# Kernel optimization log

Hardware: AMD Instinct MI355X
Metric: run time of the kernel (lower is better)

## Reference

```python
import jax, jax.numpy as jnp
import numpy as np
from jax import lax


def _lstm_dir(x_gates, Whh, bhh, reverse):
    # x_gates: (B,T,4H) = x @ Wih.T + bih, precomputed for all timesteps
    B, T, G = x_gates.shape
    H = G // 4

    def step(carry, xg):
        h, c = carry
        g = xg + h @ Whh.T + bhh
        i, f, gg, o = jnp.split(g, 4, axis=-1)  # PyTorch gate order i,f,g,o
        c = jax.nn.sigmoid(f) * c + jax.nn.sigmoid(i) * jnp.tanh(gg)
        h = jax.nn.sigmoid(o) * jnp.tanh(c)
        return (h, c), h

    xs = jnp.swapaxes(x_gates, 0, 1)  # (T,B,4H)
    if reverse:
        xs = xs[::-1]
    init = (jnp.zeros((B, H), x_gates.dtype), jnp.zeros((B, H), x_gates.dtype))
    _, hs = lax.scan(step, init, xs)
    if reverse:
        hs = hs[::-1]
    return jnp.swapaxes(hs, 0, 1)  # (B,T,H)


def _forward(embeddings, mask,
             enc_Wih_f, enc_Whh_f, enc_bih_f, enc_bhh_f,
             enc_Wih_b, enc_Whh_b, enc_bih_b, enc_bhh_b,
             attn_W, attn_b, tag_embed,
             dec_Wih, dec_Whh, dec_bih, dec_bhh,
             Wout, bout):
    B, T, D = embeddings.shape
    maskf = mask.astype(embeddings.dtype)

    # --- bidirectional encoder ---
    xg_f = jnp.einsum('btd,gd->btg', embeddings, enc_Wih_f) + enc_bih_f
    xg_b = jnp.einsum('btd,gd->btg', embeddings, enc_Wih_b) + enc_bih_b
    out_f = _lstm_dir(xg_f, enc_Whh_f, enc_bhh_f, False)
    out_b = _lstm_dir(xg_b, enc_Whh_b, enc_bhh_b, True)
    output = jnp.concatenate([out_f, out_b], axis=-1) * maskf[:, :, None]  # (B,T,2H)

    lengths = mask.sum(axis=1) - 1
    last_output = output[jnp.arange(B), lengths]  # (B,2H)

    def attend(v):
        # AllenNLP BilinearAttention: softmax(v @ W @ M^T + b), then * mask
        sc = jnp.einsum('bd,de,bte->bt', v, attn_W, output) + attn_b
        return jax.nn.softmax(sc, axis=-1) * maskf

    context0 = jnp.einsum('bt,btd->bd', attend(last_output), output)  # (B,2H)

    Hd = output.shape[-1]          # decoder hidden = 2H
    E = tag_embed.shape[1]         # tag embedding dim (== hidden_size)
    h0 = jnp.zeros((B, Hd), embeddings.dtype)
    c0 = jnp.zeros((B, Hd), embeddings.dtype)

    def step(carry, xt):
        h, c, context, last_tag = carry
        aligned, i = xt
        emb = jnp.where(i == 0,
                        jnp.zeros((B, E), embeddings.dtype),
                        tag_embed[last_tag])
        dec_input = jnp.concatenate([emb, context, aligned], axis=-1)  # (B, E+4H)
        g = dec_input @ dec_Wih.T + dec_bih + h @ dec_Whh.T + dec_bhh
        ii, f, gg, o = jnp.split(g, 4, axis=-1)
        c = jax.nn.sigmoid(f) * c + jax.nn.sigmoid(ii) * jnp.tanh(gg)
        h = jax.nn.sigmoid(o) * jnp.tanh(c)
        concated = jnp.concatenate([h, context], axis=-1)  # (B,4H)
        score = concated @ Wout.T + bout                   # (B,V)
        new_context = jnp.einsum('bt,btd->bd', attend(h), output)
        last_tag = jnp.argmax(score, axis=-1).astype(jnp.int32)
        return (h, c, new_context, last_tag), score

    xs = (jnp.swapaxes(output, 0, 1), jnp.arange(T))
    init = (h0, c0, context0, jnp.zeros((B,), jnp.int32))
    _, scores = lax.scan(step, init, xs)  # (T,B,V)
    return jnp.swapaxes(scores, 0, 1)     # (B,T,V) slot logits


def setup_inputs() -> dict:
    key = jax.random.key(0)
    B, T, D, H, E, V = 32, 64, 512, 512, 512, 2048
    H2 = 2 * H
    dec_in = E + 2 * H2  # tag_emb + context(2H) + aligned(2H)
    ks = jax.random.split(key, 20)
    s = 0.02
    f32 = jnp.float32
    return {
        'embeddings': jax.random.normal(ks[0], (B, T, D), f32),
        'mask': jnp.ones((B, T), jnp.int32),
        'enc_Wih_f': jax.random.normal(ks[1], (4 * H, D), f32) * s,
        'enc_Whh_f': jax.random.normal(ks[2], (4 * H, H), f32) * s,
        'enc_bih_f': jax.random.normal(ks[3], (4 * H,), f32) * s,
        'enc_bhh_f': jax.random.normal(ks[4], (4 * H,), f32) * s,
        'enc_Wih_b': jax.random.normal(ks[5], (4 * H, D), f32) * s,
        'enc_Whh_b': jax.random.normal(ks[6], (4 * H, H), f32) * s,
        'enc_bih_b': jax.random.normal(ks[7], (4 * H,), f32) * s,
        'enc_bhh_b': jax.random.normal(ks[8], (4 * H,), f32) * s,
        'attn_W': jax.random.normal(ks[9], (H2, H2), f32) * s,
        'attn_b': jax.random.normal(ks[10], (), f32) * s,
        'tag_embed': jax.random.normal(ks[11], (V, E), f32) * s,
        'dec_Wih': jax.random.normal(ks[12], (4 * H2, dec_in), f32) * s,
        'dec_Whh': jax.random.normal(ks[13], (4 * H2, H2), f32) * s,
        'dec_bih': jax.random.normal(ks[14], (4 * H2,), f32) * s,
        'dec_bhh': jax.random.normal(ks[15], (4 * H2,), f32) * s,
        'Wout': jax.random.normal(ks[16], (V, 2 * H2), f32) * s,
        'bout': jax.random.normal(ks[17], (V,), f32) * s,
    }


def reference(embeddings, mask,
              enc_Wih_f, enc_Whh_f, enc_bih_f, enc_bhh_f,
              enc_Wih_b, enc_Whh_b, enc_bih_b, enc_bhh_b,
              attn_W, attn_b, tag_embed,
              dec_Wih, dec_Whh, dec_bih, dec_bhh,
              Wout, bout):
    return _forward(embeddings, mask,
                    enc_Wih_f, enc_Whh_f, enc_bih_f, enc_bhh_f,
                    enc_Wih_b, enc_Whh_b, enc_bih_b, enc_bhh_b,
                    attn_W, attn_b, tag_embed,
                    dec_Wih, dec_Whh, dec_bih, dec_bhh,
                    Wout, bout)
```

## Files before the change

### kernel.cpp

```cpp
#include <hip/hip_runtime.h>

#define B   32
#define T   64
#define D   512
#define H   512
#define H2  1024
#define G4  4096
#define V   2048
#define DEC_IN 2560

__device__ __forceinline__ float sigm(float x) { return 1.f / (1.f + expf(-x)); }

__device__ __forceinline__ unsigned fenc(float f) {
  unsigned u = __float_as_uint(f);
  return (u & 0x80000000u) ? ~u : (u | 0x80000000u);
}

__device__ __forceinline__ void st_wt(float* p, float v) {
  __hip_atomic_store(p, v, __ATOMIC_RELAXED, __HIP_MEMORY_SCOPE_AGENT);
}

__device__ __forceinline__ void pbar(unsigned* slots, unsigned* flags, int myid, int nblk) {
  __syncthreads();
  if (threadIdx.x == 0)
    __hip_atomic_store(slots + myid, 1u, __ATOMIC_RELAXED, __HIP_MEMORY_SCOPE_AGENT);
  if (myid == 0) {
    for (int s = threadIdx.x; s < nblk; s += 256) {
      while (!__hip_atomic_load(slots + s, __ATOMIC_RELAXED, __HIP_MEMORY_SCOPE_AGENT))
        __builtin_amdgcn_s_sleep(1);
    }
    __syncthreads();
    if (threadIdx.x < 16)
      __hip_atomic_store(flags + threadIdx.x*16, 1u, __ATOMIC_RELAXED, __HIP_MEMORY_SCOPE_AGENT);
  }
  if (threadIdx.x == 0) {
    unsigned* f = flags + (myid & 15)*16;
    while (!__hip_atomic_load(f, __ATOMIC_RELAXED, __HIP_MEMORY_SCOPE_AGENT))
      __builtin_amdgcn_s_sleep(1);
    (void)__hip_atomic_load(f, __ATOMIC_ACQUIRE, __HIP_MEMORY_SCOPE_AGENT);
  }
  __syncthreads();
}

__device__ __forceinline__ void pbar_na(unsigned* slots, unsigned* flags, int myid, int nblk) {
  __syncthreads();
  if (threadIdx.x == 0)
    __hip_atomic_store(slots + myid, 1u, __ATOMIC_RELAXED, __HIP_MEMORY_SCOPE_AGENT);
  if (myid == 0) {
    for (int s = threadIdx.x; s < nblk; s += 256) {
      while (!__hip_atomic_load(slots + s, __ATOMIC_RELAXED, __HIP_MEMORY_SCOPE_AGENT))
        __builtin_amdgcn_s_sleep(1);
    }
    __syncthreads();
    if (threadIdx.x < 16)
      __hip_atomic_store(flags + threadIdx.x*16, 1u, __ATOMIC_RELAXED, __HIP_MEMORY_SCOPE_AGENT);
  }
  if (threadIdx.x == 0) {
    unsigned* f = flags + (myid & 15)*16;
    while (!__hip_atomic_load(f, __ATOMIC_RELAXED, __HIP_MEMORY_SCOPE_AGENT))
      __builtin_amdgcn_s_sleep(1);
  }
  __syncthreads();
}

__global__ __launch_bounds__(256) void gemm_nt(
    const float* __restrict__ A, int lda,
    const float* __restrict__ W, int ldw,
    float* __restrict__ C, int ldc,
    const float* __restrict__ bias0, const float* __restrict__ bias1,
    int K)
{
  __shared__ float As[8][132];
  __shared__ float Bs[8][132];
  const int tid = threadIdx.x;
  const int nb = blockIdx.x * 128;
  const int mb = blockIdx.y * 128;
  const int tx = tid & 15;
  const int ty = tid >> 4;
  float acc[8][8] = {};

  const int am = tid >> 1, ak = (tid & 1) * 4;
  const float* aptr = A + (size_t)(mb + am) * lda + ak;
  const float* bptr = W + (size_t)(nb + am) * ldw + ak;

  for (int k0 = 0; k0 < K; k0 += 8) {
    float4 av = *(const float4*)(aptr + k0);
    float4 bv = *(const float4*)(bptr + k0);
    As[ak+0][am] = av.x; As[ak+1][am] = av.y; As[ak+2][am] = av.z; As[ak+3][am] = av.w;
    Bs[ak+0][am] = bv.x; Bs[ak+1][am] = bv.y; Bs[ak+2][am] = bv.z; Bs[ak+3][am] = bv.w;
    __syncthreads();
    #pragma unroll
    for (int k = 0; k < 8; ++k) {
      float4 a0 = *(const float4*)&As[k][ty*8];
      float4 a1 = *(const float4*)&As[k][ty*8+4];
      float4 b0 = *(const float4*)&Bs[k][tx*8];
      float4 b1 = *(const float4*)&Bs[k][tx*8+4];
      float avv[8] = {a0.x,a0.y,a0.z,a0.w,a1.x,a1.y,a1.z,a1.w};
      float bvv[8] = {b0.x,b0.y,b0.z,b0.w,b1.x,b1.y,b1.z,b1.w};
      #pragma unroll
      for (int i = 0; i < 8; ++i)
        #pragma unroll
        for (int j = 0; j < 8; ++j)
          acc[i][j] += avv[i]*bvv[j];
    }
    __syncthreads();
  }
  float b8[8];
  #pragma unroll
  for (int j = 0; j < 8; ++j) {
    float bvv = 0.f;
    if (bias0) bvv += bias0[nb + tx*8 + j];
    if (bias1) bvv += bias1[nb + tx*8 + j];
    b8[j] = bvv;
  }
  #pragma unroll
  for (int i = 0; i < 8; ++i) {
    float4 o0, o1;
    o0.x = acc[i][0]+b8[0]; o0.y = acc[i][1]+b8[1]; o0.z = acc[i][2]+b8[2]; o0.w = acc[i][3]+b8[3];
    o1.x = acc[i][4]+b8[4]; o1.y = acc[i][5]+b8[5]; o1.z = acc[i][6]+b8[6]; o1.w = acc[i][7]+b8[7];
    size_t idx = (size_t)(mb + ty*8 + i) * ldc + nb + tx*8;
    *(float4*)&C[idx]     = o0;
    *(float4*)&C[idx + 4] = o1;
  }
}

__device__ void attend_slice(int ab, int aslice, const float* __restrict__ hvec,
                             float* __restrict__ ctxdst,
                             const float* __restrict__ outbuf, const float* __restrict__ projo,
                             const int* __restrict__ mask, float* scratch, int tid)
{
  float* scp = scratch;
  float* scv = scratch + 256;
  float* p2  = scratch + 320;
  const int tq = tid >> 2, dq = tid & 3;
  const float4* hv = (const float4*)(hvec + dq*256);
  const float4* pv = (const float4*)(projo + (size_t)(ab*T + tq)*H2 + dq*256);
  float p = 0.f;
  #pragma unroll 8
  for (int k4 = 0; k4 < 64; ++k4) {
    float4 a = hv[k4], q = pv[k4];
    p += a.x*q.x + a.y*q.y + a.z*q.z + a.w*q.w;
  }
  scp[tid] = p;
  __syncthreads();
  if (tid < 64) {
    float v = scp[tid*4] + scp[tid*4+1] + scp[tid*4+2] + scp[tid*4+3];
    float mx = v;
    #pragma unroll
    for (int d = 32; d; d >>= 1) mx = fmaxf(mx, __shfl_xor(mx, d, 64));
    float e = expf(v - mx);
    float sm = e;
    #pragma unroll
    for (int d = 32; d; d >>= 1) sm += __shfl_xor(sm, d, 64);
    scv[tid] = e * (1.f / sm) * (float)mask[ab*T + tid];
  }
  __syncthreads();
  {
    const int dl = tid & 127, th = tid >> 7;
    const int dg = aslice*128 + dl;
    float acc = 0.f;
    #pragma unroll 8
    for (int q = 0; q < 32; ++q) {
      int tt = th*32 + q;
      acc += scv[tt] * outbuf[(size_t)(ab*T + tt)*H2 + dg];
    }
    if (th == 1) p2[dl] = acc;
    __syncthreads();
    if (th == 0) st_wt(&ctxdst[dg*32 + ab], acc + p2[dl]);
  }
}

__global__ __launch_bounds__(256, 1) void encoder_persistent(
    const float* __restrict__ xg_f, const float* __restrict__ xg_b,
    const float* __restrict__ Whh_f, const float* __restrict__ Whh_b,
    const int* __restrict__ mask,
    float* __restrict__ hencT,
    float* __restrict__ outbuf,
    unsigned* __restrict__ eslots, unsigned* __restrict__ eflags)
{
  __shared__ float S_lds[9216];
  __shared__ float pacc[2048];
  __shared__ float g_lds[512];
  const int blk = blockIdx.x, tid = threadIdx.x;
  const int lane = tid & 63, wv = tid >> 6;
  const int dir = blk >> 7, nd = blk & 127;
  const int hibase = nd * 4;
  const int jj = tid & 7, kk = tid >> 3;
  const int kkl = lane >> 3;
  const float* xg  = dir ? xg_b : xg_f;
  const float* Whh = dir ? Whh_b : Whh_f;
  float* hbase = hencT + dir * 32768;
  float* Sw = S_lds + wv*2304;

  float wge[2][16];
  #pragma unroll
  for (int p = 0; p < 2; ++p) {
    int jl = jj*2 + p;
    int j = (jl>>2)*512 + hibase + (jl&3);
    #pragma unroll
    for (int sc = 0; sc < 4; ++sc)
      #pragma unroll
      for (int i = 0; i < 4; ++i)
        wge[p][sc*4+i] = Whh[(size_t)j*512 + sc*128 + i*32 + kk];
  }
  float c_reg = 0.f;
  const int lr = lane >> 1, halfc = (lane & 1) * 16;
  const int grow = (lr >> 3)*32 + 8*wv + (lr & 7);

  for (int tt = 0; tt < 64; ++tt) {
    const int t = dir ? (63 - tt) : tt;
    const float* hc = hbase + (tt & 1) * 16384;
    float* hn = hbase + ((tt + 1) & 1) * 16384;

    float a0[32], a1[32];
    #pragma unroll
    for (int q = 0; q < 32; ++q) { a0[q] = 0.f; a1[q] = 0.f; }

    float4 r0, r1, r2, r3;
    {
      const float4* p = (const float4*)(hc + grow*32 + halfc);
      r0 = p[0]; r1 = p[1]; r2 = p[2]; r3 = p[3];
      float* d = Sw + lr*36 + halfc;
      *(float4*)d = r0; *(float4*)(d+4) = r1; *(float4*)(d+8) = r2; *(float4*)(d+12) = r3;
    }
    #pragma unroll
    for (int sc = 0; sc < 4; ++sc) {
      if (sc < 3) {
        const float4* p = (const float4*)(hc + ((sc+1)*128 + grow)*32 + halfc);
        r0 = p[0]; r1 = p[1]; r2 = p[2]; r3 = p[3];
      }
      const float* Sb = Sw + (sc & 1)*1152;
      #pragma unroll
      for (int i = 0; i < 4; ++i) {
        const float* sp = Sb + (i*8 + kkl)*36;
        float w0 = wge[0][sc*4+i], w1 = wge[1][sc*4+i];
        #pragma unroll
        for (int q = 0; q < 8; ++q) {
          float4 s4 = *(const float4*)(sp + q*4);
          a0[q*4+0] += w0*s4.x; a0[q*4+1] += w0*s4.y; a0[q*4+2] += w0*s4.z; a0[q*4+3] += w0*s4.w;
          a1[q*4+0] += w1*s4.x; a1[q*4+1] += w1*s4.y; a1[q*4+2] += w1*s4.z; a1[q*4+3] += w1*s4.w;
        }
      }
      if (sc < 3) {
        float* d = Sw + ((sc+1) & 1)*1152 + lr*36 + halfc;
        *(float4*)d = r0; *(float4*)(d+4) = r1; *(float4*)(d+8) = r2; *(float4*)(d+12) = r3;
      }
    }
    #pragma unroll
    for (int dd = 8; dd <= 32; dd <<= 1) {
      #pragma unroll
      for (int q = 0; q < 32; ++q) {
        a0[q] += __shfl_down(a0[q], dd, 64);
        a1[q] += __shfl_down(a1[q], dd, 64);
      }
    }
    if (lane < 8) {
      float* pw = &pacc[wv*512 + lane*64];
      #pragma unroll
      for (int q = 0; q < 32; ++q) { pw[q] = a0[q]; pw[32+q] = a1[q]; }
    }
    __syncthreads();
    #pragma unroll
    for (int r = 0; r < 2; ++r) {
      int o = tid + r*256;
      int jl = o >> 5, b = o & 31;
      int off = (jl>>1)*64 + (jl&1)*32 + b;
      float v = pacc[off] + pacc[512+off] + pacc[1024+off] + pacc[1536+off];
      v += xg[(size_t)(b*T + t)*2048 + (jl>>2)*512 + hibase + (jl&3)];
      g_lds[jl*32 + b] = v;
    }
    __syncthreads();
    if (tid < 128) {
      int hil = tid >> 5, b = tid & 31;
      float gi = g_lds[(0*4+hil)*32 + b];
      float gf = g_lds[(1*4+hil)*32 + b];
      float gg = g_lds[(2*4+hil)*32 + b];
      float go = g_lds[(3*4+hil)*32 + b];
      c_reg = sigm(gf)*c_reg + sigm(gi)*tanhf(gg);
      float h = sigm(go)*tanhf(c_reg);
      int hi = hibase + hil;
      st_wt(&hn[hi*32 + b], h);
      st_wt(&outbuf[(size_t)(b*T + t)*H2 + dir*512 + hi], h * (float)mask[b*T + t]);
    }
    pbar(eslots + (dir*64 + tt)*128, eflags + (dir*64 + tt)*256, nd, 128);
  }
}

#define GROW1(lr) (8*wv + ((lr) < 8 ? (lr) : 24 + (lr)))
#define GROW2(lr) (16*wv + (lr))
#define SLDG(qq, s) { int krr = (s)*64 + GROW1(lrow); \
  const float* bs = (krr < 1024) ? (hTc + krr*32) : (ctxc + (krr-1024)*32); \
  qq##a = *(const float4*)(bs + scol2); qq##b = *(const float4*)(bs + scol2 + 4); }
#define SLDS(qq, s) { int krr = (s)*64 + GROW2(lrow); \
  const float* bs = (krr < 1024) ? (hTn + krr*32) : (ctxc + (krr-1024)*32); \
  qq##a = *(const float4*)(bs + scol2); qq##b = *(const float4*)(bs + scol2 + 4); }
#define STW(qq, BUF) { float* d = Sw + (BUF)*576 + lrow*36 + scol2; \
  *(float4*)d = qq##a; *(float4*)(d+4) = qq##b; }
#define COMPG(sl, BUF) { const float* Sb = Sw + (BUF)*576; \
  _Pragma("unroll") for (int i = 0; i < 2; ++i) { \
    float w0 = Wg[jl0*2052 + (sl)*64 + i*32 + kkg]; \
    float w1 = Wg[jl1*2052 + (sl)*64 + i*32 + kkg]; \
    const float* sp = Sb + (i*8 + kkl)*36; \
    _Pragma("unroll") for (int q = 0; q < 8; ++q) { \
      float4 s4 = *(const float4*)(sp + q*4); \
      a0[q*4+0] += w0*s4.x; a0[q*4+1] += w0*s4.y; a0[q*4+2] += w0*s4.z; a0[q*4+3] += w0*s4.w; \
      a1[q*4+0] += w1*s4.x; a1[q*4+1] += w1*s4.y; a1[q*4+2] += w1*s4.z; a1[q*4+3] += w1*s4.w; } } }
#define COMPS(sl, BUF) { const float* sp = Sw + (BUF)*576 + lrow*36; \
  float w0 = ws0[sl], w1 = ws1[sl]; \
  _Pragma("unroll") for (int q = 0; q < 8; ++q) { \
    float4 s4 = *(const float4*)(sp + q*4); \
    a0[q*4+0] += w0*s4.x; a0[q*4+1] += w0*s4.y; a0[q*4+2] += w0*s4.z; a0[q*4+3] += w0*s4.w; \
    a1[q*4+0] += w1*s4.x; a1[q*4+1] += w1*s4.y; a1[q*4+2] += w1*s4.z; a1[q*4+3] += w1*s4.w; } }

__global__ __launch_bounds__(256, 1) void decoder_persistent(
    const float* __restrict__ basep, const float* __restrict__ tagp,
    const float* __restrict__ dWhh,  const float* __restrict__ dWih,
    const float* __restrict__ Wout,  const float* __restrict__ bout,
    const float* __restrict__ projo, const float* __restrict__ outbuf,
    const int* __restrict__ mask,
    float* __restrict__ hbufs,
    float* __restrict__ cbufs,
    float* __restrict__ rbufs,
    const float* __restrict__ zeroh,
    unsigned long long* __restrict__ argslot,
    unsigned* __restrict__ dslots, unsigned* __restrict__ dflags,
    float* __restrict__ out)
{
  extern __shared__ float dyn[];
  float* Wg    = dyn;
  float* S2    = dyn + 32832;
  float* pacc  = dyn + 37440;
  float* g_lds = dyn + 39488;

  const int blk = blockIdx.x, tid = threadIdx.x;
  const int lane = tid & 63, wv = tid >> 6;
  const int hibase = blk * 4;
  const int jj = lane & 7, kkl = lane >> 3;
  const int kkg = 8*wv + kkl;
  const int jl0 = jj*2, jl1 = jj*2 + 1;
  const int vv = tid & 3, kq = tid >> 2;
  const int vbase = blk * 8;
  const int lrow = lane >> 2, scol2 = (lane & 3) * 8;
  const int ab = blk & 31, aslice = blk >> 5;
  float* Sw = S2 + wv*1152;

  for (int jl = 0; jl < 16; ++jl) {
    int j = (jl>>2)*1024 + hibase + (jl&3);
    #pragma unroll
    for (int r = 0; r < 2; ++r) {
      int c = tid*4 + r*1024;
      float4 w;
      if (c < 1024) w = *(const float4*)(dWhh + (size_t)j*1024 + c);
      else          w = *(const float4*)(dWih + (size_t)j*2560 + 512 + (c - 1024));
      *(float4*)&Wg[jl*2052 + c] = w;
    }
  }
  float ws0[32], ws1[32];
  {
    int v0 = vbase + vv*2;
    #pragma unroll
    for (int s2 = 0; s2 < 32; ++s2) {
      ws0[s2] = Wout[(size_t)(v0+0)*2048 + s2*64 + kq];
      ws1[s2] = Wout[(size_t)(v0+1)*2048 + s2*64 + kq];
    }
  }

  float c_reg = 0.f;
  int bslot = 0;

  {
    int len = -1;
    for (int i = 0; i < T; ++i) len += mask[ab*T + i];
    attend_slice(ab, aslice, outbuf + (size_t)(ab*T + len)*H2, cbufs,
                 outbuf, projo, mask, pacc, tid);
  }
  pbar_na(dslots + (bslot)*256, dflags + (bslot)*256, blk, 256); bslot++;

  for (int t = 0; t < T; ++t) {
    const float* hTc  = (t == 0) ? zeroh : (hbufs + (size_t)(t-1)*32768);
    float*       hTn  = hbufs + (size_t)t*32768;
    const float* ctxc = cbufs + (size_t)t*32768;
    float*       ctxn = cbufs + (size_t)(t+1)*32768;
    float*       hrw  = rbufs + (size_t)t*32768;

    const int b_own = tid & 31;
    const int jlA = tid >> 5, jlB = jlA + 8;
    const int jA = (jlA>>2)*1024 + hibase + (jlA&3);
    const int jB = (jlB>>2)*1024 + hibase + (jlB&3);
    float extA = basep[(size_t)(b_own*T + t)*G4 + jA];
    float extB = basep[(size_t)(b_own*T + t)*G4 + jB];
    if (t > 0) {
      unsigned long long sl64 = __hip_atomic_load(&argslot[((t+2)%3)*32 + b_own],
                                                  __ATOMIC_RELAXED, __HIP_MEMORY_SCOPE_AGENT);
      unsigned tg = ~(unsigned)sl64;
      extA += tagp[(size_t)tg*G4 + jA];
      extB += tagp[(size_t)tg*G4 + jB];
    }

    float a0[32], a1[32];
    #pragma unroll
    for (int q = 0; q < 32; ++q) { a0[q] = 0.f; a1[q] = 0.f; }
    {
      float4 q0a,q0b,q1a,q1b,q2a,q2b,q3a,q3b;
      SLDG(q0, 0) SLDG(q1, 1) SLDG(q2, 2) SLDG(q3, 3)
      STW(q0, 0)
      for (int g = 0; g < 8; ++g) {
        const int sl = g*4;
        if (sl+4 < 32) SLDG(q0, sl+4)
        COMPG(sl, 0)
        STW(q1, 1)
        if (sl+5 < 32) SLDG(q1, sl+5)
        COMPG(sl+1, 1)
        STW(q2, 0)
        if (sl+6 < 32) SLDG(q2, sl+6)
        COMPG(sl+2, 0)
        STW(q3, 1)
        if (sl+7 < 32) SLDG(q3, sl+7)
        COMPG(sl+3, 1)
        if (sl+4 < 32) STW(q0, 0)
      }
    }
    #pragma unroll
    for (int dd = 8; dd <= 32; dd <<= 1) {
      #pragma unroll
      for (int q = 0; q < 32; ++q) {
        a0[q] += __shfl_down(a0[q], dd, 64);
        a1[q] += __shfl_down(a1[q], dd, 64);
      }
    }
    if (lane < 8) {
      float* pw = &pacc[wv*512 + lane*64];
      #pragma unroll
      for (int q = 0; q < 32; ++q) { pw[q] = a0[q]; pw[32+q] = a1[q]; }
    }
    __syncthreads();
    #pragma unroll
    for (int r = 0; r < 2; ++r) {
      int o = tid + r*256;
      int jl = o >> 5, b = o & 31;
      int off = (jl>>1)*64 + (jl&1)*32 + b;
      float vsum = pacc[off] + pacc[512+off] + pacc[1024+off] + pacc[1536+off];
      vsum += (r == 0) ? extA : extB;
      g_lds[jl*32 + b] = vsum;
    }
    __syncthreads();
    if (tid < 128) {
      int hil = tid >> 5, b = tid & 31;
      float gi = g_lds[(0*4+hil)*32 + b];
      float gf = g_lds[(1*4+hil)*32 + b];
      float gg = g_lds[(2*4+hil)*32 + b];
      float go = g_lds[(3*4+hil)*32 + b];
      c_reg = sigm(gf)*c_reg + sigm(gi)*tanhf(gg);
      float h = sigm(go)*tanhf(c_reg);
      int hi = hibase + hil;
      st_wt(&hTn[hi*32 + b], h);
      st_wt(&hrw[b*1024 + hi], h);
    }
    pbar_na(dslots + (bslot)*256, dflags + (bslot)*256, blk, 256); bslot++;

    #pragma unroll
    for (int q = 0; q < 32; ++q) { a0[q] = 0.f; a1[q] = 0.f; }
    {
      float4 q0a,q0b,q1a,q1b,q2a,q2b,q3a,q3b;
      SLDS(q0, 0) SLDS(q1, 1) SLDS(q2, 2) SLDS(q3, 3)
      STW(q0, 0)
      #pragma unroll
      for (int g = 0; g < 8; ++g) {
        const int sl = g*4;
        if (sl+4 < 32) SLDS(q0, sl+4)
        COMPS(sl, 0)
        STW(q1, 1)
        if (sl+5 < 32) SLDS(q1, sl+5)
        COMPS(sl+1, 1)
        STW(q2, 0)
        if (sl+6 < 32) SLDS(q2, sl+6)
        COMPS(sl+2, 0)
        STW(q3, 1)
        if (sl+7 < 32) SLDS(q3, sl+7)
        COMPS(sl+3, 1)
        if (sl+4 < 32) STW(q0, 0)
      }
    }
    #pragma unroll
    for (int dd = 4; dd <= 32; dd <<= 1) {
      #pragma unroll
      for (int q = 0; q < 32; ++q) {
        a0[q] += __shfl_down(a0[q], dd, 64);
        a1[q] += __shfl_down(a1[q], dd, 64);
      }
    }
    if (lane < 4) {
      float* pw = &pacc[wv*256 + lane*64];
      #pragma unroll
      for (int q = 0; q < 32; ++q) { pw[q] = a0[q]; pw[32+q] = a1[q]; }
    }
    __syncthreads();
    {
      int vl = tid & 7, b = tid >> 3;
      int off = (vl>>1)*64 + (vl&1)*32 + b;
      float s = pacc[off] + pacc[256+off] + pacc[512+off] + pacc[768+off];
      s += bout[vbase + vl];
      st_wt(&out[(size_t)(b*T + t)*V + vbase + vl], s);
      g_lds[vl*32 + b] = s;
    }
    __syncthreads();
    if (tid < 32) {
      int b = tid;
      float best = g_lds[b]; int bi = 0;
      #pragma unroll
      for (int vl = 1; vl < 8; ++vl) {
        float s = g_lds[vl*32 + b];
        if (s > best) { best = s; bi = vl; }
      }
      unsigned long long e = ((unsigned long long)fenc(best) << 32)
                           | (unsigned long long)(unsigned)(~(unsigned)(vbase + bi));
      atomicMax(&argslot[(t%3)*32 + b], e);
    } else if (blk == 0 && tid >= 32 && tid < 64) {
      __hip_atomic_store(&argslot[((t+1)%3)*32 + (tid - 32)], 0ull,
                         __ATOMIC_RELAXED, __HIP_MEMORY_SCOPE_AGENT);
    }
    if (t < 63) {
      __syncthreads();
      attend_slice(ab, aslice, hrw + ab*1024, ctxn, outbuf, projo, mask, pacc, tid);
    }
    pbar_na(dslots + (bslot)*256, dflags + (bslot)*256, blk, 256); bslot++;
  }
}

extern "C" void kernel_launch(void* const* d_in, const int* in_sizes, int n_in,
                              void* d_out, int out_size, void* d_ws, size_t ws_size,
                              hipStream_t stream)
{
  (void)in_sizes; (void)n_in; (void)out_size; (void)ws_size;
  const float* emb    = (const float*)d_in[0];
  const int*   mask   = (const int*)d_in[1];
  const float* Wih_f  = (const float*)d_in[2];
  const float* Whh_f  = (const float*)d_in[3];
  const float* bih_f  = (const float*)d_in[4];
  const float* bhh_f  = (const float*)d_in[5];
  const float* Wih_b  = (const float*)d_in[6];
  const float* Whh_b  = (const float*)d_in[7];
  const float* bih_b  = (const float*)d_in[8];
  const float* bhh_b  = (const float*)d_in[9];
  const float* attnW  = (const float*)d_in[10];
  const float* tagemb = (const float*)d_in[12];
  const float* dWih   = (const float*)d_in[13];
  const float* dWhh   = (const float*)d_in[14];
  const float* dbih   = (const float*)d_in[15];
  const float* dbhh   = (const float*)d_in[16];
  const float* Wout   = (const float*)d_in[17];
  const float* bout   = (const float*)d_in[18];
  float* out = (float*)d_out;

  float* ws = (float*)d_ws;
  float* xg_f   = ws + 0;
  float* xg_b   = ws + 4194304;
  float* hbufs  = ws + 0;
  float* cbufs  = ws + 2097152;
  float* rbufs  = ws + 4227072;
  float* outbuf = ws + 8388608;
  float* projo  = ws + 10485760;
  float* basep  = ws + 12582912;
  float* tagp   = ws + 20971520;
  float* zeroh  = ws + 29360128;
  float* hencT  = ws + 29523968;
  unsigned long long* argslot = (unsigned long long*)(ws + 29589504);
  unsigned* dslots = (unsigned*)(ws + 29589696);
  unsigned* dflags = (unsigned*)(ws + 29622720);
  unsigned* eslots = (unsigned*)(ws + 29655744);
  unsigned* eflags = (unsigned*)(ws + 29672128);

  (void)hipFuncSetAttribute((const void*)decoder_persistent,
                            hipFuncAttributeMaxDynamicSharedMemorySize, 160000);

  hipMemsetAsync((void*)(ws + 29360128), 0, (size_t)(29704896 - 29360128) * sizeof(float), stream);

  gemm_nt<<<dim3(16, 16), 256, 0, stream>>>(emb, 512, Wih_f, 512, xg_f, 2048, bih_f, bhh_f, 512);
  gemm_nt<<<dim3(16, 16), 256, 0, stream>>>(emb, 512, Wih_b, 512, xg_b, 2048, bih_b, bhh_b, 512);
  gemm_nt<<<dim3(32, 16), 256, 0, stream>>>(tagemb, 512, dWih, DEC_IN, tagp, G4, nullptr, nullptr, 512);
  encoder_persistent<<<256, 256, 0, stream>>>(xg_f, xg_b, Whh_f, Whh_b, mask, hencT, outbuf, eslots, eflags);
  gemm_nt<<<dim3(8, 16), 256, 0, stream>>>(outbuf, H2, attnW, H2, projo, H2, nullptr, nullptr, H2);
  gemm_nt<<<dim3(32, 16), 256, 0, stream>>>(outbuf, H2, dWih + 1536, DEC_IN, basep, G4, dbih, dbhh, H2);
  decoder_persistent<<<256, 256, 160000, stream>>>(basep, tagp, dWhh, dWih, Wout, bout,
                                                   projo, outbuf, mask, hbufs, cbufs, rbufs, zeroh,
                                                   argslot, dslots, dflags, out);
}
```

Before: 4.548 ms.

## Use per-timestep encoder hidden buffers with non-acquire barrier; prefetch GEMM tiles

The encoder now writes each timestep's hidden state into its own buffer instead of ping-ponging between two. That removes write-after-read hazards, which lets the grid barrier drop its acquire load (pbar_na). Separately, the tiled GEMM register-prefetches the next K slice while computing the current one, hiding global load latency. The per-timestep buffers reuse the basep region, which is only written after the encoder finishes. They also use more memory and rely on the weaker barrier still ordering the relaxed atomic stores correctly.

```diff
diff --git a/kernel.cpp b/kernel.cpp
--- a/kernel.cpp
+++ b/kernel.cpp
@@ -18,28 +18,6 @@
 
 __device__ __forceinline__ void st_wt(float* p, float v) {
   __hip_atomic_store(p, v, __ATOMIC_RELAXED, __HIP_MEMORY_SCOPE_AGENT);
-}
-
-__device__ __forceinline__ void pbar(unsigned* slots, unsigned* flags, int myid, int nblk) {
-  __syncthreads();
-  if (threadIdx.x == 0)
-    __hip_atomic_store(slots + myid, 1u, __ATOMIC_RELAXED, __HIP_MEMORY_SCOPE_AGENT);
-  if (myid == 0) {
-    for (int s = threadIdx.x; s < nblk; s += 256) {
-      while (!__hip_atomic_load(slots + s, __ATOMIC_RELAXED, __HIP_MEMORY_SCOPE_AGENT))
-        __builtin_amdgcn_s_sleep(1);
-    }
-    __syncthreads();
-    if (threadIdx.x < 16)
-      __hip_atomic_store(flags + threadIdx.x*16, 1u, __ATOMIC_RELAXED, __HIP_MEMORY_SCOPE_AGENT);
-  }
-  if (threadIdx.x == 0) {
-    unsigned* f = flags + (myid & 15)*16;
-    while (!__hip_atomic_load(f, __ATOMIC_RELAXED, __HIP_MEMORY_SCOPE_AGENT))
-      __builtin_amdgcn_s_sleep(1);
-    (void)__hip_atomic_load(f, __ATOMIC_ACQUIRE, __HIP_MEMORY_SCOPE_AGENT);
-  }
-  __syncthreads();
 }
 
 __device__ __forceinline__ void pbar_na(unsigned* slots, unsigned* flags, int myid, int nblk) {
@@ -83,12 +61,17 @@
   const float* aptr = A + (size_t)(mb + am) * lda + ak;
   const float* bptr = W + (size_t)(nb + am) * ldw + ak;
 
+  float4 av = *(const float4*)(aptr);
+  float4 bv = *(const float4*)(bptr);
   for (int k0 = 0; k0 < K; k0 += 8) {
-    float4 av = *(const float4*)(aptr + k0);
-    float4 bv = *(const float4*)(bptr + k0);
     As[ak+0][am] = av.x; As[ak+1][am] = av.y; As[ak+2][am] = av.z; As[ak+3][am] = av.w;
     Bs[ak+0][am] = bv.x; Bs[ak+1][am] = bv.y; Bs[ak+2][am] = bv.z; Bs[ak+3][am] = bv.w;
     __syncthreads();
+    float4 avn = av, bvn = bv;
+    if (k0 + 8 < K) {
+      avn = *(const float4*)(aptr + k0 + 8);
+      bvn = *(const float4*)(bptr + k0 + 8);
+    }
     #pragma unroll
     for (int k = 0; k < 8; ++k) {
       float4 a0 = *(const float4*)&As[k][ty*8];
@@ -104,6 +87,7 @@
           acc[i][j] += avv[i]*bvv[j];
     }
     __syncthreads();
+    av = avn; bv = bvn;
   }
   float b8[8];
   #pragma unroll
@@ -174,7 +158,8 @@
     const float* __restrict__ xg_f, const float* __restrict__ xg_b,
     const float* __restrict__ Whh_f, const float* __restrict__ Whh_b,
     const int* __restrict__ mask,
-    float* __restrict__ hencT,
+    float* __restrict__ hebufs,
+    const float* __restrict__ zeroh,
     float* __restrict__ outbuf,
     unsigned* __restrict__ eslots, unsigned* __restrict__ eflags)
 {
@@ -189,7 +174,7 @@
   const int kkl = lane >> 3;
   const float* xg  = dir ? xg_b : xg_f;
   const float* Whh = dir ? Whh_b : Whh_f;
-  float* hbase = hencT + dir * 32768;
+  float* hebase = hebufs + (size_t)dir * 1048576;
   float* Sw = S_lds + wv*2304;
 
   float wge[2][16];
@@ -209,8 +194,8 @@
 
   for (int tt = 0; tt < 64; ++tt) {
     const int t = dir ? (63 - tt) : tt;
-    const float* hc = hbase + (tt & 1) * 16384;
-    float* hn = hbase + ((tt + 1) & 1) * 16384;
+    const float* hc = tt ? (hebase + (size_t)(tt-1)*16384) : zeroh;
+    float* hn = hebase + (size_t)tt*16384;
 
     float a0[32], a1[32];
     #pragma unroll
@@ -282,7 +267,7 @@
       st_wt(&hn[hi*32 + b], h);
       st_wt(&outbuf[(size_t)(b*T + t)*H2 + dir*512 + hi], h * (float)mask[b*T + t]);
     }
-    pbar(eslots + (dir*64 + tt)*128, eflags + (dir*64 + tt)*256, nd, 128);
+    pbar_na(eslots + (dir*64 + tt)*128, eflags + (dir*64 + tt)*256, nd, 128);
   }
 }
 
@@ -561,9 +546,9 @@
   float* outbuf = ws + 8388608;
   float* projo  = ws + 10485760;
   float* basep  = ws + 12582912;
+  float* hebufs = ws + 12582912;
   float* tagp   = ws + 20971520;
   float* zeroh  = ws + 29360128;
-  float* hencT  = ws + 29523968;
   unsigned long long* argslot = (unsigned long long*)(ws + 29589504);
   unsigned* dslots = (unsigned*)(ws + 29589696);
   unsigned* dflags = (unsigned*)(ws + 29622720);
@@ -578,7 +563,8 @@
   gemm_nt<<<dim3(16, 16), 256, 0, stream>>>(emb, 512, Wih_f, 512, xg_f, 2048, bih_f, bhh_f, 512);
   gemm_nt<<<dim3(16, 16), 256, 0, stream>>>(emb, 512, Wih_b, 512, xg_b, 2048, bih_b, bhh_b, 512);
   gemm_nt<<<dim3(32, 16), 256, 0, stream>>>(tagemb, 512, dWih, DEC_IN, tagp, G4, nullptr, nullptr, 512);
-  encoder_persistent<<<256, 256, 0, stream>>>(xg_f, xg_b, Whh_f, Whh_b, mask, hencT, outbuf, eslots, eflags);
+  encoder_persistent<<<256, 256, 0, stream>>>(xg_f, xg_b, Whh_f, Whh_b, mask,
+                                              hebufs, zeroh, outbuf, eslots, eflags);
   gemm_nt<<<dim3(8, 16), 256, 0, stream>>>(outbuf, H2, attnW, H2, projo, H2, nullptr, nullptr, H2);
   gemm_nt<<<dim3(32, 16), 256, 0, stream>>>(outbuf, H2, dWih + 1536, DEC_IN, basep, G4, dbih, dbhh, H2);
   decoder_persistent<<<256, 256, 160000, stream>>>(basep, tagp, dWhh, dWih, Wout, bout,
```

New measurement: 4.414 ms (median of 2 runs). 3.0% less time.
